# Performance work log

Hardware: AMD Instinct MI355X
Metric: run time of the kernel (lower is better)

## Reference

```python
import jax, jax.numpy as jnp
import numpy as np

B, NF, QUERY_DIM = 4, 300, 512
HIDDEN, NUM_HEADS = 512, 8
H, W = 80, 80
HEAD_DIM = HIDDEN // NUM_HEADS
NORM_FACT = float(HIDDEN / NUM_HEADS) ** (-0.5)


def setup_inputs() -> dict:
    key = jax.random.key(0)
    k1, k2, k3, k4, k5 = jax.random.split(key, 5)
    # xavier_uniform bound for [HIDDEN, QUERY_DIM] weight
    bound = float(np.sqrt(6.0 / (HIDDEN + QUERY_DIM)))
    return {
        "q": jax.random.normal(k1, (B, NF, QUERY_DIM), dtype=jnp.float32),
        "k": jax.random.normal(k2, (B, QUERY_DIM, H, W), dtype=jnp.float32),
        "mask": jax.random.bernoulli(k3, 0.25, (B, H, W)),  # True = masked out
        "q_w": jax.random.uniform(k4, (HIDDEN, QUERY_DIM), jnp.float32, -bound, bound),
        "q_b": jnp.zeros((HIDDEN,), jnp.float32),
        "k_w": jax.random.uniform(k5, (HIDDEN, QUERY_DIM), jnp.float32, -bound, bound),
        "k_b": jnp.zeros((HIDDEN,), jnp.float32),
    }


def reference(q, k, mask, q_w, q_b, k_w, k_b):
    b, nf, _ = q.shape
    h, w = k.shape[-2], k.shape[-1]
    # q projection: [b, nf, hidden]
    qp = jnp.einsum("bqd,ed->bqe", q, q_w) + q_b
    # k projection (1x1 conv == channel matmul): [b, hidden, h, w]
    kp = jnp.einsum("bdhw,ed->behw", k, k_w) + k_b[None, :, None, None]
    # split heads
    qh = qp.reshape(b, nf, NUM_HEADS, HEAD_DIM) * NORM_FACT   # [b,q,n,c]
    kh = kp.reshape(b, NUM_HEADS, HEAD_DIM, h, w)             # [b,n,c,h,w]
    # batched QK scores (replaces the per-query python loop + cat(dim=2))
    weights = jnp.einsum("bqnc,bnchw->bqnhw", qh, kh)
    weights = weights.reshape(b, 1, nf * NUM_HEADS, h, w)
    # masked_fill with -inf on padded spatial positions
    weights = jnp.where(mask[:, None, None, :, :], -jnp.inf, weights)
    # NOTE: softmax over flatten(2) = jointly over (queries*heads*h*w), as in source
    weights = jax.nn.softmax(weights.reshape(b, 1, -1), axis=-1)
    return weights.reshape(b, 1, nf * NUM_HEADS, h, w)
```

## Files before the change

### kernel.cpp

```cpp
#include <hip/hip_runtime.h>
#include <math.h>

#define B_    4
#define NF    300
#define QD    512
#define HID   512
#define NH    8
#define HD    64
#define HW    6400
#define ROWS  2400
#define PB    15360000
#define NORM_FACT 0.125f
#define NEG_INF (-INFINITY)
#define LDK   40

typedef __bf16 bf16_t;
typedef __bf16 bf16x4_t __attribute__((ext_vector_type(4)));
typedef __bf16 bf16x8_t __attribute__((ext_vector_type(8)));
typedef float  f32x4    __attribute__((ext_vector_type(4)));

__device__ __forceinline__ void splitf(float x, bf16_t& h, bf16_t& l) {
    h = (bf16_t)x;
    l = (bf16_t)(x - (float)h);
}

__global__ __launch_bounds__(256) void qproj_kernel(
    const float* __restrict__ q, const float* __restrict__ qw,
    const float* __restrict__ qb, float* __restrict__ qh)
{
    __shared__ float qs[4][QD];
    const int r0 = blockIdx.x * 4;
    const int t  = threadIdx.x;
    #pragma unroll
    for (int row = 0; row < 4; ++row) {
        qs[row][t]       = q[(size_t)(r0 + row) * QD + t];
        qs[row][t + 256] = q[(size_t)(r0 + row) * QD + t + 256];
    }
    __syncthreads();
    #pragma unroll
    for (int eo = 0; eo < 2; ++eo) {
        const int e = t + eo * 256;
        float a0 = 0.f, a1 = 0.f, a2 = 0.f, a3 = 0.f;
        for (int d = 0; d < QD; d += 4) {
            float4 w = *(const float4*)&qw[(size_t)e * QD + d];
            a0 += qs[0][d]*w.x + qs[0][d+1]*w.y + qs[0][d+2]*w.z + qs[0][d+3]*w.w;
            a1 += qs[1][d]*w.x + qs[1][d+1]*w.y + qs[1][d+2]*w.z + qs[1][d+3]*w.w;
            a2 += qs[2][d]*w.x + qs[2][d+1]*w.y + qs[2][d+2]*w.z + qs[2][d+3]*w.w;
            a3 += qs[3][d]*w.x + qs[3][d+1]*w.y + qs[3][d+2]*w.z + qs[3][d+3]*w.w;
        }
        const float bias = qb[e];
        qh[(size_t)(r0+0)*HID + e] = (a0 + bias) * NORM_FACT;
        qh[(size_t)(r0+1)*HID + e] = (a1 + bias) * NORM_FACT;
        qh[(size_t)(r0+2)*HID + e] = (a2 + bias) * NORM_FACT;
        qh[(size_t)(r0+3)*HID + e] = (a3 + bias) * NORM_FACT;
    }
}

__global__ __launch_bounds__(256) void kproj_mfma(
    const float* __restrict__ k, const float* __restrict__ kw,
    const float* __restrict__ kb, float* __restrict__ kp)
{
    __shared__ __align__(16) bf16_t Ah[128][LDK];
    __shared__ __align__(16) bf16_t Al[128][LDK];
    __shared__ __align__(16) bf16_t Bh[128][LDK];
    __shared__ __align__(16) bf16_t Bl[128][LDK];
    const int b  = blockIdx.z;
    const int e0 = blockIdx.y * 128;
    const int p0 = blockIdx.x * 128;
    const int t  = threadIdx.x;
    const int wave = t >> 6, lane = t & 63;
    const int wr = wave >> 1, wc = wave & 1;
    const int lm = lane & 15, lq = lane >> 4;
    const float* kB = k + (size_t)b * QD * HW;

    f32x4 acc[4][4];
    const f32x4 zero4 = {0.f, 0.f, 0.f, 0.f};
    #pragma unroll
    for (int i = 0; i < 4; ++i)
        #pragma unroll
        for (int j = 0; j < 4; ++j) acc[i][j] = zero4;

    for (int d0 = 0; d0 < QD; d0 += 32) {
        #pragma unroll
        for (int i = 0; i < 4; ++i) {
            int idx = t + i * 256;
            int e = idx >> 3, dp = (idx & 7) << 2;
            float4 v = *(const float4*)&kw[(size_t)(e0 + e) * QD + d0 + dp];
            bf16x4_t hv, lv; bf16_t hx, lx;
            splitf(v.x, hx, lx); hv[0] = hx; lv[0] = lx;
            splitf(v.y, hx, lx); hv[1] = hx; lv[1] = lx;
            splitf(v.z, hx, lx); hv[2] = hx; lv[2] = lx;
            splitf(v.w, hx, lx); hv[3] = hx; lv[3] = lx;
            *(bf16x4_t*)&Ah[e][dp] = hv;
            *(bf16x4_t*)&Al[e][dp] = lv;
        }
        #pragma unroll
        for (int i = 0; i < 4; ++i) {
            int idx = t + i * 256;
            int p = idx & 127, db = (idx >> 7) << 2;
            bf16x4_t hv, lv;
            #pragma unroll
            for (int j = 0; j < 4; ++j) {
                float x = kB[(size_t)(d0 + db + j) * HW + p0 + p];
                bf16_t hx, lx; splitf(x, hx, lx);
                hv[j] = hx; lv[j] = lx;
            }
            *(bf16x4_t*)&Bh[p][db] = hv;
            *(bf16x4_t*)&Bl[p][db] = lv;
        }
        __syncthreads();

        bf16x8_t ah[4], al[4], bh[4], bl[4];
        #pragma unroll
        for (int mt = 0; mt < 4; ++mt) {
            int r = wr * 64 + mt * 16 + lm;
            ah[mt] = *(const bf16x8_t*)&Ah[r][lq * 8];
            al[mt] = *(const bf16x8_t*)&Al[r][lq * 8];
        }
        #pragma unroll
        for (int nt = 0; nt < 4; ++nt) {
            int c = wc * 64 + nt * 16 + lm;
            bh[nt] = *(const bf16x8_t*)&Bh[c][lq * 8];
            bl[nt] = *(const bf16x8_t*)&Bl[c][lq * 8];
        }
        #pragma unroll
        for (int mt = 0; mt < 4; ++mt)
            #pragma unroll
            for (int nt = 0; nt < 4; ++nt) {
                f32x4 a = acc[mt][nt];
                a = __builtin_amdgcn_mfma_f32_16x16x32_bf16(al[mt], bh[nt], a, 0, 0, 0);
                a = __builtin_amdgcn_mfma_f32_16x16x32_bf16(ah[mt], bl[nt], a, 0, 0, 0);
                a = __builtin_amdgcn_mfma_f32_16x16x32_bf16(ah[mt], bh[nt], a, 0, 0, 0);
                acc[mt][nt] = a;
            }
        __syncthreads();
    }

    #pragma unroll
    for (int mt = 0; mt < 4; ++mt) {
        #pragma unroll
        for (int reg = 0; reg < 4; ++reg) {
            int e = e0 + wr * 64 + mt * 16 + lq * 4 + reg;
            float bias = kb[e];
            float* dst = kp + (size_t)b * HID * HW + (size_t)e * HW + p0 + wc * 64 + lm;
            #pragma unroll
            for (int nt = 0; nt < 4; ++nt)
                dst[nt * 16] = acc[mt][nt][reg] + bias;
        }
    }
}

__global__ __launch_bounds__(256) void scores_mfma(
    const float* __restrict__ qh, const float* __restrict__ kp,
    const int* __restrict__ mask, float* __restrict__ out,
    float* __restrict__ partials)
{
    __shared__ __align__(16) bf16_t Ah[128][LDK];
    __shared__ __align__(16) bf16_t Al[128][LDK];
    __shared__ __align__(16) bf16_t Bh[128][LDK];
    __shared__ __align__(16) bf16_t Bl[128][LDK];
    const int z  = blockIdx.z;
    const int b  = z >> 3, n = z & 7;
    const int q0 = blockIdx.y * 128;
    const int p0 = blockIdx.x * 128;
    const int t  = threadIdx.x;
    const int wave = t >> 6, lane = t & 63;
    const int wr = wave >> 1, wc = wave & 1;
    const int lm = lane & 15, lq = lane >> 4;

    f32x4 acc[4][4];
    const f32x4 zero4 = {0.f, 0.f, 0.f, 0.f};
    #pragma unroll
    for (int i = 0; i < 4; ++i)
        #pragma unroll
        for (int j = 0; j < 4; ++j) acc[i][j] = zero4;

    for (int d0 = 0; d0 < HD; d0 += 32) {
        #pragma unroll
        for (int i = 0; i < 4; ++i) {
            int idx = t + i * 256;
            int qq = idx >> 3, dp = (idx & 7) << 2;
            int qg = q0 + qq;
            float4 v = make_float4(0.f, 0.f, 0.f, 0.f);
            if (qg < NF)
                v = *(const float4*)&qh[(size_t)(b * NF + qg) * HID + n * HD + d0 + dp];
            bf16x4_t hv, lv; bf16_t hx, lx;
            splitf(v.x, hx, lx); hv[0] = hx; lv[0] = lx;
            splitf(v.y, hx, lx); hv[1] = hx; lv[1] = lx;
            splitf(v.z, hx, lx); hv[2] = hx; lv[2] = lx;
            splitf(v.w, hx, lx); hv[3] = hx; lv[3] = lx;
            *(bf16x4_t*)&Ah[qq][dp] = hv;
            *(bf16x4_t*)&Al[qq][dp] = lv;
        }
        const float* kpB = kp + (size_t)b * HID * HW + (size_t)(n * HD + d0) * HW;
        #pragma unroll
        for (int i = 0; i < 4; ++i) {
            int idx = t + i * 256;
            int p = idx & 127, db = (idx >> 7) << 2;
            bf16x4_t hv, lv;
            #pragma unroll
            for (int j = 0; j < 4; ++j) {
                float x = kpB[(size_t)(db + j) * HW + p0 + p];
                bf16_t hx, lx; splitf(x, hx, lx);
                hv[j] = hx; lv[j] = lx;
            }
            *(bf16x4_t*)&Bh[p][db] = hv;
            *(bf16x4_t*)&Bl[p][db] = lv;
        }
        __syncthreads();

        bf16x8_t ah[4], al[4], bh[4], bl[4];
        #pragma unroll
        for (int mt = 0; mt < 4; ++mt) {
            int r = wr * 64 + mt * 16 + lm;
            ah[mt] = *(const bf16x8_t*)&Ah[r][lq * 8];
            al[mt] = *(const bf16x8_t*)&Al[r][lq * 8];
        }
        #pragma unroll
        for (int nt = 0; nt < 4; ++nt) {
            int c = wc * 64 + nt * 16 + lm;
            bh[nt] = *(const bf16x8_t*)&Bh[c][lq * 8];
            bl[nt] = *(const bf16x8_t*)&Bl[c][lq * 8];
        }
        #pragma unroll
        for (int mt = 0; mt < 4; ++mt)
            #pragma unroll
            for (int nt = 0; nt < 4; ++nt) {
                f32x4 a = acc[mt][nt];
                a = __builtin_amdgcn_mfma_f32_16x16x32_bf16(al[mt], bh[nt], a, 0, 0, 0);
                a = __builtin_amdgcn_mfma_f32_16x16x32_bf16(ah[mt], bl[nt], a, 0, 0, 0);
                a = __builtin_amdgcn_mfma_f32_16x16x32_bf16(ah[mt], bh[nt], a, 0, 0, 0);
                acc[mt][nt] = a;
            }
        __syncthreads();
    }

    int mm[4];
    #pragma unroll
    for (int nt = 0; nt < 4; ++nt)
        mm[nt] = mask[b * HW + p0 + wc * 64 + nt * 16 + lm];

    float tm = NEG_INF;
    #pragma unroll
    for (int mt = 0; mt < 4; ++mt) {
        int qbase = q0 + wr * 64 + mt * 16 + lq * 4;
        #pragma unroll
        for (int reg = 0; reg < 4; ++reg) {
            if (qbase + reg < NF) {
                #pragma unroll
                for (int nt = 0; nt < 4; ++nt)
                    if (!mm[nt]) tm = fmaxf(tm, acc[mt][nt][reg]);
            }
        }
    }
    float ts = 0.f;
    if (tm != NEG_INF) {
        #pragma unroll
        for (int mt = 0; mt < 4; ++mt) {
            int qbase = q0 + wr * 64 + mt * 16 + lq * 4;
            #pragma unroll
            for (int reg = 0; reg < 4; ++reg) {
                if (qbase + reg < NF) {
                    #pragma unroll
                    for (int nt = 0; nt < 4; ++nt)
                        if (!mm[nt]) ts += __expf(acc[mt][nt][reg] - tm);
                }
            }
        }
    }

    #pragma unroll
    for (int mt = 0; mt < 4; ++mt) {
        #pragma unroll
        for (int reg = 0; reg < 4; ++reg) {
            int qg = q0 + wr * 64 + mt * 16 + lq * 4 + reg;
            if (qg < NF) {
                float* dst = out + (size_t)(b * ROWS + qg * NH + n) * HW + p0 + wc * 64 + lm;
                #pragma unroll
                for (int nt = 0; nt < 4; ++nt)
                    dst[nt * 16] = mm[nt] ? NEG_INF : acc[mt][nt][reg];
            }
        }
    }

    float* redM = (float*)&Ah[0][0];
    float* redS = redM + 256;
    redM[t] = tm; redS[t] = ts;
    __syncthreads();
    for (int off = 128; off > 0; off >>= 1) {
        if (t < off) {
            float m1 = redM[t],       s1 = redS[t];
            float m2 = redM[t + off], s2 = redS[t + off];
            float M = fmaxf(m1, m2);
            float s = (M == NEG_INF) ? 0.f
                      : (s1 * __expf(m1 - M) + s2 * __expf(m2 - M));
            redM[t] = M; redS[t] = s;
        }
        __syncthreads();
    }
    if (t == 0) {
        int lin = (z * gridDim.y + blockIdx.y) * gridDim.x + blockIdx.x;
        partials[2 * lin]     = redM[0];
        partials[2 * lin + 1] = redS[0];
    }
}

__global__ __launch_bounds__(256) void stats_kernel(
    const float* __restrict__ partials, float* __restrict__ stats, int nper)
{
    __shared__ float redM[256];
    __shared__ float redS[256];
    const int b = blockIdx.x, t = threadIdx.x;
    const float* p = partials + (size_t)b * nper * 2;
    float m = NEG_INF, s = 0.f;
    for (int i = t; i < nper; i += 256) {
        float m2 = p[2 * i], s2 = p[2 * i + 1];
        float M = fmaxf(m, m2);
        float ns = (M == NEG_INF) ? 0.f
                   : (s * __expf(m - M) + s2 * __expf(m2 - M));
        m = M; s = ns;
    }
    redM[t] = m; redS[t] = s;
    __syncthreads();
    for (int off = 128; off > 0; off >>= 1) {
        if (t < off) {
            float m1 = redM[t],       s1 = redS[t];
            float m2 = redM[t + off], s2 = redS[t + off];
            float M = fmaxf(m1, m2);
            float ns = (M == NEG_INF) ? 0.f
                       : (s1 * __expf(m1 - M) + s2 * __expf(m2 - M));
            redM[t] = M; redS[t] = ns;
        }
        __syncthreads();
    }
    if (t == 0) {
        stats[2 * b]     = redM[0];
        stats[2 * b + 1] = 1.0f / redS[0];
    }
}

__global__ __launch_bounds__(256) void norm_kernel(
    float* __restrict__ out, const float* __restrict__ stats)
{
    const int i4 = blockIdx.x * 256 + threadIdx.x;
    if (i4 >= (B_ * PB) / 4) return;
    const int b = i4 / (PB / 4);
    const float M    = stats[2 * b];
    const float invS = stats[2 * b + 1];
    float4 v = ((const float4*)out)[i4];
    v.x = __expf(v.x - M) * invS;
    v.y = __expf(v.y - M) * invS;
    v.z = __expf(v.z - M) * invS;
    v.w = __expf(v.w - M) * invS;
    ((float4*)out)[i4] = v;
}

extern "C" void kernel_launch(void* const* d_in, const int* in_sizes, int n_in,
                              void* d_out, int out_size, void* d_ws, size_t ws_size,
                              hipStream_t stream) {
    const float* q    = (const float*)d_in[0];
    const float* k    = (const float*)d_in[1];
    const int*   mask = (const int*)  d_in[2];
    const float* qw   = (const float*)d_in[3];
    const float* qb   = (const float*)d_in[4];
    const float* kw   = (const float*)d_in[5];
    const float* kb   = (const float*)d_in[6];
    float* out = (float*)d_out;
    float* ws  = (float*)d_ws;

    float* qh       = ws;
    float* kp       = ws + 614400;
    float* partials = ws + 13721600;
    float* stats    = ws + 13731200;

    qproj_kernel<<<300, 256, 0, stream>>>(q, qw, qb, qh);
    kproj_mfma<<<dim3(50, 4, 4), 256, 0, stream>>>(k, kw, kb, kp);
    scores_mfma<<<dim3(50, 3, 32), 256, 0, stream>>>(qh, kp, mask, out, partials);
    stats_kernel<<<4, 256, 0, stream>>>(partials, stats, 1200);
    norm_kernel<<<60000, 256, 0, stream>>>(out, stats);
}
```

Baseline: 563.4 us.

## Recompute scores in two passes instead of writing and renormalizing the output

```diff
diff --git a/kernel.cpp b/kernel.cpp
--- a/kernel.cpp
+++ b/kernel.cpp
@@ -150,15 +150,14 @@
     }
 }
 
-__global__ __launch_bounds__(256) void scores_mfma(
+__global__ __launch_bounds__(256) void scores_pass_a(
     const float* __restrict__ qh, const float* __restrict__ kp,
-    const int* __restrict__ mask, float* __restrict__ out,
-    float* __restrict__ partials)
+    const int* __restrict__ mask, float* __restrict__ partials)
 {
     __shared__ __align__(16) bf16_t Ah[128][LDK];
-    __shared__ __align__(16) bf16_t Al[128][LDK];
     __shared__ __align__(16) bf16_t Bh[128][LDK];
-    __shared__ __align__(16) bf16_t Bl[128][LDK];
+    __shared__ float redM[256];
+    __shared__ float redS[256];
     const int z  = blockIdx.z;
     const int b  = z >> 3, n = z & 7;
     const int q0 = blockIdx.y * 128;
@@ -184,54 +183,37 @@
             float4 v = make_float4(0.f, 0.f, 0.f, 0.f);
             if (qg < NF)
                 v = *(const float4*)&qh[(size_t)(b * NF + qg) * HID + n * HD + d0 + dp];
-            bf16x4_t hv, lv; bf16_t hx, lx;
-            splitf(v.x, hx, lx); hv[0] = hx; lv[0] = lx;
-            splitf(v.y, hx, lx); hv[1] = hx; lv[1] = lx;
-            splitf(v.z, hx, lx); hv[2] = hx; lv[2] = lx;
-            splitf(v.w, hx, lx); hv[3] = hx; lv[3] = lx;
+            bf16x4_t hv;
+            hv[0] = (bf16_t)v.x; hv[1] = (bf16_t)v.y;
+            hv[2] = (bf16_t)v.z; hv[3] = (bf16_t)v.w;
             *(bf16x4_t*)&Ah[qq][dp] = hv;
-            *(bf16x4_t*)&Al[qq][dp] = lv;
         }
         const float* kpB = kp + (size_t)b * HID * HW + (size_t)(n * HD + d0) * HW;
         #pragma unroll
         for (int i = 0; i < 4; ++i) {
             int idx = t + i * 256;
             int p = idx & 127, db = (idx >> 7) << 2;
-            bf16x4_t hv, lv;
-            #pragma unroll
-            for (int j = 0; j < 4; ++j) {
-                float x = kpB[(size_t)(db + j) * HW + p0 + p];
-                bf16_t hx, lx; splitf(x, hx, lx);
-                hv[j] = hx; lv[j] = lx;
-            }
+            bf16x4_t hv;
+            #pragma unroll
+            for (int j = 0; j < 4; ++j)
+                hv[j] = (bf16_t)kpB[(size_t)(db + j) * HW + p0 + p];
             *(bf16x4_t*)&Bh[p][db] = hv;
-            *(bf16x4_t*)&Bl[p][db] = lv;
-        }
-        __syncthreads();
-
-        bf16x8_t ah[4], al[4], bh[4], bl[4];
-        #pragma unroll
-        for (int mt = 0; mt < 4; ++mt) {
-            int r = wr * 64 + mt * 16 + lm;
-            ah[mt] = *(const bf16x8_t*)&Ah[r][lq * 8];
-            al[mt] = *(const bf16x8_t*)&Al[r][lq * 8];
-        }
-        #pragma unroll
-        for (int nt = 0; nt < 4; ++nt) {
-            int c = wc * 64 + nt * 16 + lm;
-            bh[nt] = *(const bf16x8_t*)&Bh[c][lq * 8];
-            bl[nt] = *(const bf16x8_t*)&Bl[c][lq * 8];
-        }
+        }
+        __syncthreads();
+
+        bf16x8_t ah[4], bh[4];
         #pragma unroll
         for (int mt = 0; mt < 4; ++mt)
-            #pragma unroll
-            for (int nt = 0; nt < 4; ++nt) {
-                f32x4 a = acc[mt][nt];
-                a = __builtin_amdgcn_mfma_f32_16x16x32_bf16(al[mt], bh[nt], a, 0, 0, 0);
-                a = __builtin_amdgcn_mfma_f32_16x16x32_bf16(ah[mt], bl[nt], a, 0, 0, 0);
-                a = __builtin_amdgcn_mfma_f32_16x16x32_bf16(ah[mt], bh[nt], a, 0, 0, 0);
-                acc[mt][nt] = a;
-            }
+            ah[mt] = *(const bf16x8_t*)&Ah[wr * 64 + mt * 16 + lm][lq * 8];
+        #pragma unroll
+        for (int nt = 0; nt < 4; ++nt)
+            bh[nt] = *(const bf16x8_t*)&Bh[wc * 64 + nt * 16 + lm][lq * 8];
+        #pragma unroll
+        for (int mt = 0; mt < 4; ++mt)
+            #pragma unroll
+            for (int nt = 0; nt < 4; ++nt)
+                acc[mt][nt] = __builtin_amdgcn_mfma_f32_16x16x32_bf16(
+                    ah[mt], bh[nt], acc[mt][nt], 0, 0, 0);
         __syncthreads();
     }
 
@@ -269,22 +251,6 @@
         }
     }
 
-    #pragma unroll
-    for (int mt = 0; mt < 4; ++mt) {
-        #pragma unroll
-        for (int reg = 0; reg < 4; ++reg) {
-            int qg = q0 + wr * 64 + mt * 16 + lq * 4 + reg;
-            if (qg < NF) {
-                float* dst = out + (size_t)(b * ROWS + qg * NH + n) * HW + p0 + wc * 64 + lm;
-                #pragma unroll
-                for (int nt = 0; nt < 4; ++nt)
-                    dst[nt * 16] = mm[nt] ? NEG_INF : acc[mt][nt][reg];
-            }
-        }
-    }
-
-    float* redM = (float*)&Ah[0][0];
-    float* redS = redM + 256;
     redM[t] = tm; redS[t] = ts;
     __syncthreads();
     for (int off = 128; off > 0; off >>= 1) {
@@ -339,20 +305,112 @@
     }
 }
 
-__global__ __launch_bounds__(256) void norm_kernel(
-    float* __restrict__ out, const float* __restrict__ stats)
+__global__ __launch_bounds__(256) void scores_pass_b(
+    const float* __restrict__ qh, const float* __restrict__ kp,
+    const int* __restrict__ mask, const float* __restrict__ stats,
+    float* __restrict__ out)
 {
-    const int i4 = blockIdx.x * 256 + threadIdx.x;
-    if (i4 >= (B_ * PB) / 4) return;
-    const int b = i4 / (PB / 4);
+    __shared__ __align__(16) bf16_t Ah[128][LDK];
+    __shared__ __align__(16) bf16_t Al[128][LDK];
+    __shared__ __align__(16) bf16_t Bh[128][LDK];
+    __shared__ __align__(16) bf16_t Bl[128][LDK];
+    const int z  = blockIdx.z;
+    const int b  = z >> 3, n = z & 7;
+    const int q0 = blockIdx.y * 128;
+    const int p0 = blockIdx.x * 128;
+    const int t  = threadIdx.x;
+    const int wave = t >> 6, lane = t & 63;
+    const int wr = wave >> 1, wc = wave & 1;
+    const int lm = lane & 15, lq = lane >> 4;
+
     const float M    = stats[2 * b];
     const float invS = stats[2 * b + 1];
-    float4 v = ((const float4*)out)[i4];
-    v.x = __expf(v.x - M) * invS;
-    v.y = __expf(v.y - M) * invS;
-    v.z = __expf(v.z - M) * invS;
-    v.w = __expf(v.w - M) * invS;
-    ((float4*)out)[i4] = v;
+
+    f32x4 acc[4][4];
+    const f32x4 zero4 = {0.f, 0.f, 0.f, 0.f};
+    #pragma unroll
+    for (int i = 0; i < 4; ++i)
+        #pragma unroll
+        for (int j = 0; j < 4; ++j) acc[i][j] = zero4;
+
+    for (int d0 = 0; d0 < HD; d0 += 32) {
+        #pragma unroll
+        for (int i = 0; i < 4; ++i) {
+            int idx = t + i * 256;
+            int qq = idx >> 3, dp = (idx & 7) << 2;
+            int qg = q0 + qq;
+            float4 v = make_float4(0.f, 0.f, 0.f, 0.f);
+            if (qg < NF)
+                v = *(const float4*)&qh[(size_t)(b * NF + qg) * HID + n * HD + d0 + dp];
+            bf16x4_t hv, lv; bf16_t hx, lx;
+            splitf(v.x, hx, lx); hv[0] = hx; lv[0] = lx;
+            splitf(v.y, hx, lx); hv[1] = hx; lv[1] = lx;
+            splitf(v.z, hx, lx); hv[2] = hx; lv[2] = lx;
+            splitf(v.w, hx, lx); hv[3] = hx; lv[3] = lx;
+            *(bf16x4_t*)&Ah[qq][dp] = hv;
+            *(bf16x4_t*)&Al[qq][dp] = lv;
+        }
+        const float* kpB = kp + (size_t)b * HID * HW + (size_t)(n * HD + d0) * HW;
+        #pragma unroll
+        for (int i = 0; i < 4; ++i) {
+            int idx = t + i * 256;
+            int p = idx & 127, db = (idx >> 7) << 2;
+            bf16x4_t hv, lv;
+            #pragma unroll
+            for (int j = 0; j < 4; ++j) {
+                float x = kpB[(size_t)(db + j) * HW + p0 + p];
+                bf16_t hx, lx; splitf(x, hx, lx);
+                hv[j] = hx; lv[j] = lx;
+            }
+            *(bf16x4_t*)&Bh[p][db] = hv;
+            *(bf16x4_t*)&Bl[p][db] = lv;
+        }
+        __syncthreads();
+
+        bf16x8_t ah[4], al[4], bh[4], bl[4];
+        #pragma unroll
+        for (int mt = 0; mt < 4; ++mt) {
+            int r = wr * 64 + mt * 16 + lm;
+            ah[mt] = *(const bf16x8_t*)&Ah[r][lq * 8];
+            al[mt] = *(const bf16x8_t*)&Al[r][lq * 8];
+        }
+        #pragma unroll
+        for (int nt = 0; nt < 4; ++nt) {
+            int c = wc * 64 + nt * 16 + lm;
+            bh[nt] = *(const bf16x8_t*)&Bh[c][lq * 8];
+            bl[nt] = *(const bf16x8_t*)&Bl[c][lq * 8];
+        }
+        #pragma unroll
+        for (int mt = 0; mt < 4; ++mt)
+            #pragma unroll
+            for (int nt = 0; nt < 4; ++nt) {
+                f32x4 a = acc[mt][nt];
+                a = __builtin_amdgcn_mfma_f32_16x16x32_bf16(al[mt], bh[nt], a, 0, 0, 0);
+                a = __builtin_amdgcn_mfma_f32_16x16x32_bf16(ah[mt], bl[nt], a, 0, 0, 0);
+                a = __builtin_amdgcn_mfma_f32_16x16x32_bf16(ah[mt], bh[nt], a, 0, 0, 0);
+                acc[mt][nt] = a;
+            }
+        __syncthreads();
+    }
+
+    int mm[4];
+    #pragma unroll
+    for (int nt = 0; nt < 4; ++nt)
+        mm[nt] = mask[b * HW + p0 + wc * 64 + nt * 16 + lm];
+
+    #pragma unroll
+    for (int mt = 0; mt < 4; ++mt) {
+        #pragma unroll
+        for (int reg = 0; reg < 4; ++reg) {
+            int qg = q0 + wr * 64 + mt * 16 + lq * 4 + reg;
+            if (qg < NF) {
+                float* dst = out + (size_t)(b * ROWS + qg * NH + n) * HW + p0 + wc * 64 + lm;
+                #pragma unroll
+                for (int nt = 0; nt < 4; ++nt)
+                    dst[nt * 16] = mm[nt] ? 0.f : __expf(acc[mt][nt][reg] - M) * invS;
+            }
+        }
+    }
 }
 
 extern "C" void kernel_launch(void* const* d_in, const int* in_sizes, int n_in,
@@ -375,7 +433,7 @@
 
     qproj_kernel<<<300, 256, 0, stream>>>(q, qw, qb, qh);
     kproj_mfma<<<dim3(50, 4, 4), 256, 0, stream>>>(k, kw, kb, kp);
-    scores_mfma<<<dim3(50, 3, 32), 256, 0, stream>>>(qh, kp, mask, out, partials);
+    scores_pass_a<<<dim3(50, 3, 32), 256, 0, stream>>>(qh, kp, mask, partials);
     stats_kernel<<<4, 256, 0, stream>>>(partials, stats, 1200);
-    norm_kernel<<<60000, 256, 0, stream>>>(out, stats);
-}
+    scores_pass_b<<<dim3(50, 3, 32), 256, 0, stream>>>(qh, kp, mask, stats, out);
+}
```

New measurement: 505.9 us. -10.2%, faster.
